# Kernel optimization log

Measured on AMD Instinct MI355X. Metric: run time of the kernel, lower is better.

The kernel has to match this reference:

```python
import jax, jax.numpy as jnp
import numpy as np

T = 8
TAU = 2.0
V_TH = 1.0
ALPHA = 2.0  # ATan surrogate alpha (spikingjelly default)

@jax.custom_vjp
def spike_fn(x):
    # Heaviside forward, ATan surrogate backward
    return (x >= 0.0).astype(x.dtype)

def _spike_fwd(x):
    return spike_fn(x), x

def _spike_bwd(x, g):
    sg = (ALPHA / 2.0) / (1.0 + (jnp.pi / 2.0 * ALPHA * x) ** 2)
    return (g * sg,)

spike_fn.defvjp(_spike_fwd, _spike_bwd)

def lif_scan(currents):
    """LIF over time. currents: (T, B, D). tau=2, v_reset=0 (hard), decay_input=True, detach_reset=True."""
    v0 = jnp.zeros(currents.shape[1:], currents.dtype)
    def step(v, x):
        v = v + (x - v) / TAU            # charge with input decay
        s = spike_fn(v - V_TH)           # fire
        sd = jax.lax.stop_gradient(s)    # detach_reset=True
        v = v * (1.0 - sd)               # hard reset to v_reset=0
        return v, s
    _, spikes = jax.lax.scan(step, v0, currents)
    return spikes  # (T, B, D)

def _linear(x, W, b):
    # x: (T,B,I), W: (O,I) torch layout
    return jnp.einsum('tbi,oi->tbo', x, W) + b

def setup_inputs() -> dict:
    key = jax.random.key(0)
    ks = jax.random.split(key, 9)
    B, D_in, D_out = 32768, 128, 64
    def lin(k, o, i):
        k1, k2 = jax.random.split(k)
        bound = 1.0 / np.sqrt(i)
        W = jax.random.uniform(k1, (o, i), jnp.float32, -bound, bound)
        b = jax.random.uniform(k2, (o,), jnp.float32, -bound, bound)
        return W, b
    W1, b1 = lin(ks[1], 256, D_in)
    W2, b2 = lin(ks[2], 128, 256)
    W3, b3 = lin(ks[3], 64, 128)
    W4, b4 = lin(ks[4], D_out, 64)
    x = jax.random.normal(ks[0], (B, D_in), jnp.float32)
    return {"x": x, "W1": W1, "b1": b1, "W2": W2, "b2": b2,
            "W3": W3, "b3": b3, "W4": W4, "b4": b4}

def reference(x, W1, b1, W2, b2, W3, b3, W4, b4):
    # Poisson rate coding: bernoulli(sigmoid(x)) per timestep (fixed key => deterministic)
    p = jax.nn.sigmoid(x)
    enc_key = jax.random.key(42)
    spikes_in = jax.random.bernoulli(enc_key, p, (T,) + x.shape).astype(x.dtype)  # (T,B,128)
    h = lif_scan(_linear(spikes_in, W1, b1))
    h = lif_scan(_linear(h, W2, b2))
    h = lif_scan(_linear(h, W3, b3))
    out = _linear(h, W4, b4)  # (T,B,64)
    return out.mean(axis=0)   # (B,64)
```

## Files before the change

kernel.cpp:

```cpp
#include <hip/hip_runtime.h>
#include <hip/hip_bf16.h>
#include <stdint.h>
#include <math.h>

#define TT 8

typedef __attribute__((ext_vector_type(8))) short short8;
typedef __attribute__((ext_vector_type(4))) float f32x4;

__device__ __forceinline__ uint16_t bf16_rne(float f) {
  uint32_t u = __float_as_uint(f);
  return (uint16_t)((u + 0x7fffu + ((u >> 16) & 1u)) >> 16);
}
__device__ __forceinline__ float bf16_f32(uint16_t b) {
  return __uint_as_float((uint32_t)b << 16);
}

__device__ __forceinline__ uint32_t rotl32(uint32_t v, int r) {
#if __has_builtin(__builtin_amdgcn_alignbit)
  return __builtin_amdgcn_alignbit(v, v, 32 - r);
#else
  return (v << r) | (v >> (32 - r));
#endif
}

__device__ __forceinline__ void tf_0_42(uint32_t x0, uint32_t x1,
                                        uint32_t& o0, uint32_t& o1) {
  const uint32_t K1 = 42u, KS2 = 0x1BD11BDAu ^ 42u;
  uint32_t v0 = x0;
  uint32_t v1 = x1 + K1;
#define R4(a,b,c,d) \
  v0 += v1; v1 = rotl32(v1, a); v1 ^= v0; \
  v0 += v1; v1 = rotl32(v1, b); v1 ^= v0; \
  v0 += v1; v1 = rotl32(v1, c); v1 ^= v0; \
  v0 += v1; v1 = rotl32(v1, d); v1 ^= v0;
  R4(13, 15, 26, 6)   v0 += K1;  v1 += KS2 + 1u;
  R4(17, 29, 16, 24)  v0 += KS2; v1 += 2u;
  R4(13, 15, 26, 6)    v1 += K1 + 3u;
  R4(17, 29, 16, 24)  v0 += K1;  v1 += KS2 + 4u;
  R4(13, 15, 26, 6)   v0 += KS2; v1 += 5u;
#undef R4
  o0 = v0; o1 = v1;
}

__device__ __forceinline__ void threefry2x32(uint32_t k0, uint32_t k1,
                                             uint32_t x0, uint32_t x1,
                                             uint32_t& o0, uint32_t& o1) {
  const uint32_t ks2 = 0x1BD11BDAu ^ k0 ^ k1;
  uint32_t v0 = x0 + k0, v1 = x1 + k1;
#define TFR(r) { v0 += v1; v1 = rotl32(v1, r); v1 ^= v0; }
  TFR(13) TFR(15) TFR(26) TFR(6)   v0 += k1;  v1 += ks2 + 1u;
  TFR(17) TFR(29) TFR(16) TFR(24)  v0 += ks2; v1 += k0 + 2u;
  TFR(13) TFR(15) TFR(26) TFR(6)   v0 += k0;  v1 += k1 + 3u;
  TFR(17) TFR(29) TFR(16) TFR(24)  v0 += k1;  v1 += ks2 + 4u;
  TFR(13) TFR(15) TFR(26) TFR(6)   v0 += ks2; v1 += k0 + 5u;
#undef TFR
  o0 = v0; o1 = v1;
}

__device__ __forceinline__ bool bern_lt(uint32_t bits, float p32, float xv) {
  const float u = __uint_as_float((bits >> 9) | 0x3f800000u) - 1.0f;
  const float d = u - p32;
  if (__builtin_expect(fabsf(d) < 8e-6f, 0)) {
    const double p = 1.0 / (1.0 + exp(-(double)xv));
    return (double)u < p;
  }
  return d < 0.0f;
}

__global__ void __launch_bounds__(256)
w1split_kernel(const float* __restrict__ W1, uint16_t* __restrict__ W1s)
{
  const int gid = blockIdx.x * 256 + threadIdx.x;
  const int j = gid & 7, nt = (gid >> 3) & 1, lane = (gid >> 4) & 63;
  const int sp = (gid >> 10) & 3, nc = gid >> 12;
  const int k = sp * 32 + (lane >> 4) * 8 + j;
  const int n = nc * 32 + nt * 16 + (lane & 15);
  W1s[gid] = bf16_rne(W1[n * 128 + k]);
}

__global__ void __launch_bounds__(256, 4)
snn_k1(const float* __restrict__ x, const uint16_t* __restrict__ W1s,
       const float* __restrict__ B1, const float* __restrict__ B4,
       uint32_t* __restrict__ s1g, uint32_t* __restrict__ flgg,
       float* __restrict__ out)
{
  __shared__ __align__(16) uint8_t sbits[128 * 16];
  __shared__ float bias_s[256];
  __shared__ uint16_t s1t[128 * 16];
  __shared__ uint32_t exc;

  const int tid = threadIdx.x;
  const int lane = tid & 63, wid = tid >> 6, g = lane >> 4;

  for (int i = tid; i < 1024; i += 256) ((uint32_t*)s1t)[i] = 0;
  if (tid == 0) exc = 0;
  bias_s[tid] = B1[tid];

  {
    const int b = tid >> 4, w8 = tid & 15;
    const int gb = blockIdx.x * 16 + b;
    float xv[8];
    *(float4*)&xv[0] = *(const float4*)&x[(size_t)gb * 128 + w8 * 8];
    *(float4*)&xv[4] = *(const float4*)&x[(size_t)gb * 128 + w8 * 8 + 4];
    const uint32_t ebase = ((uint32_t)gb << 7) | (uint32_t)(w8 * 8);
    uint32_t m[TT] = {0, 0, 0, 0, 0, 0, 0, 0};
    uint32_t ambig = 0;
    #pragma unroll
    for (int j = 0; j < 8; ++j) {
      const float p1 = 1.0f + 1.0f / (1.0f + expf(-xv[j]));
      #pragma unroll
      for (int t = 0; t < 4; ++t) {
        const uint32_t e = ebase + (uint32_t)j + ((uint32_t)t << 22);
        uint32_t o0, o1;
        tf_0_42(e, e + 0x01000000u, o0, o1);
        const float d0 = __uint_as_float((o0 >> 9) | 0x3f800000u) - p1;
        const float d1 = __uint_as_float((o1 >> 9) | 0x3f800000u) - p1;
        m[t]     |= (d0 < 0.0f ? 1u : 0u) << j;
        m[t + 4] |= (d1 < 0.0f ? 1u : 0u) << j;
        ambig |= ((fabsf(d0) < 1e-5f) || (fabsf(d1) < 1e-5f)) ? (1u << j) : 0u;
      }
    }
    if (__builtin_expect(ambig != 0u, 0)) {
      for (int j = 0; j < 8; ++j) {
        if ((ambig >> j) & 1u) {
          const double p = 1.0 / (1.0 + exp(-(double)xv[j]));
          for (int t = 0; t < 4; ++t) {
            const uint32_t e = ebase + (uint32_t)j + ((uint32_t)t << 22);
            uint32_t o0, o1;
            tf_0_42(e, e + 0x01000000u, o0, o1);
            const float u0 = __uint_as_float((o0 >> 9) | 0x3f800000u) - 1.0f;
            const float u1 = __uint_as_float((o1 >> 9) | 0x3f800000u) - 1.0f;
            m[t]     = (m[t]     & ~(1u << j)) | (((double)u0 < p ? 1u : 0u) << j);
            m[t + 4] = (m[t + 4] & ~(1u << j)) | (((double)u1 < p ? 1u : 0u) << j);
          }
        }
      }
    }
    #pragma unroll
    for (int t = 0; t < TT; ++t)
      sbits[(b * 8 + t) * 16 + w8] = (uint8_t)m[t];
  }
  __syncthreads();

  short8 a0_0, a0_1, a0_2, a0_3, a1_0, a1_1, a1_2, a1_3;
  {
    const uint8_t* rp0 = &sbits[(wid * 32 + (lane & 15)) * 16];
    const uint8_t* rp1 = rp0 + 256;
#define MKFRAG(dst, rp, s) { \
    const uint32_t byte = (rp)[(s) * 4 + g]; \
    short8 a; \
    a[0] = (short)((byte & 1u)   ? 0x3F80 : 0); \
    a[1] = (short)((byte & 2u)   ? 0x3F80 : 0); \
    a[2] = (short)((byte & 4u)   ? 0x3F80 : 0); \
    a[3] = (short)((byte & 8u)   ? 0x3F80 : 0); \
    a[4] = (short)((byte & 16u)  ? 0x3F80 : 0); \
    a[5] = (short)((byte & 32u)  ? 0x3F80 : 0); \
    a[6] = (short)((byte & 64u)  ? 0x3F80 : 0); \
    a[7] = (short)((byte & 128u) ? 0x3F80 : 0); \
    dst = a; }
    MKFRAG(a0_0, rp0, 0) MKFRAG(a0_1, rp0, 1) MKFRAG(a0_2, rp0, 2) MKFRAG(a0_3, rp0, 3)
    MKFRAG(a1_0, rp1, 0) MKFRAG(a1_1, rp1, 1) MKFRAG(a1_2, rp1, 2) MKFRAG(a1_3, rp1, 3)
#undef MKFRAG
  }

  const uint8_t* wlane = (const uint8_t*)W1s + lane * 32;

  #pragma unroll 1
  for (int nc = 0; nc < 8; ++nc) {
    const uint8_t* wnc = wlane + nc * 8192;
    f32x4 C00 = {0.f, 0.f, 0.f, 0.f};
    f32x4 C01 = C00, C10 = C00, C11 = C00;
    short8 bf0, bf1;
#define STEP(sp, A0, A1) \
    bf0 = *(const short8*)(wnc + (sp) * 2048); \
    bf1 = *(const short8*)(wnc + (sp) * 2048 + 16); \
    C00 = __builtin_amdgcn_mfma_f32_16x16x32_bf16(A0, bf0, C00, 0, 0, 0); \
    C10 = __builtin_amdgcn_mfma_f32_16x16x32_bf16(A1, bf0, C10, 0, 0, 0); \
    C01 = __builtin_amdgcn_mfma_f32_16x16x32_bf16(A0, bf1, C01, 0, 0, 0); \
    C11 = __builtin_amdgcn_mfma_f32_16x16x32_bf16(A1, bf1, C11, 0, 0, 0);
    STEP(0, a0_0, a1_0) STEP(1, a0_1, a1_1) STEP(2, a0_2, a1_2) STEP(3, a0_3, a1_3)
#undef STEP

#define EPI(Cv, mi, nt) { \
    const float bbv = bias_s[nc * 32 + (nt) * 16 + (lane & 15)]; \
    const float cr0 = Cv[0] + bbv, cr1 = Cv[1] + bbv; \
    const float cr2 = Cv[2] + bbv, cr3 = Cv[3] + bbv; \
    float u = cr0 * 0.5f; \
    float mx = u; \
    u = (u + cr1) * 0.5f; mx = fmaxf(mx, u); \
    u = (u + cr2) * 0.5f; mx = fmaxf(mx, u); \
    u = (u + cr3) * 0.5f; mx = fmaxf(mx, u); \
    const float u3o = __shfl_xor(u, 16); \
    const float ub = (g & 1) ? mx + fmaxf(u3o, 0.f) * 0.5f : mx; \
    if (__any(ub >= 1.0f)) { \
      float v = 0.f; uint32_t nib = 0; \
      { const float vn = (v + cr0) * 0.5f; const bool s = vn >= 1.0f; nib |= s ? 1u : 0u; v = s ? 0.f : vn; } \
      { const float vn = (v + cr1) * 0.5f; const bool s = vn >= 1.0f; nib |= s ? 2u : 0u; v = s ? 0.f : vn; } \
      { const float vn = (v + cr2) * 0.5f; const bool s = vn >= 1.0f; nib |= s ? 4u : 0u; v = s ? 0.f : vn; } \
      { const float vn = (v + cr3) * 0.5f; const bool s = vn >= 1.0f; nib |= s ? 8u : 0u; v = s ? 0.f : vn; } \
      const float v3 = __shfl_xor(v, 16); \
      if (g & 1) { \
        v = v3; nib = 0; \
        { const float vn = (v + cr0) * 0.5f; const bool s = vn >= 1.0f; nib |= s ? 1u : 0u; v = s ? 0.f : vn; } \
        { const float vn = (v + cr1) * 0.5f; const bool s = vn >= 1.0f; nib |= s ? 2u : 0u; v = s ? 0.f : vn; } \
        { const float vn = (v + cr2) * 0.5f; const bool s = vn >= 1.0f; nib |= s ? 4u : 0u; v = s ? 0.f : vn; } \
        { const float vn = (v + cr3) * 0.5f; const bool s = vn >= 1.0f; nib |= s ? 8u : 0u; v = s ? 0.f : vn; } \
      } \
      _Pragma("unroll") \
      for (int r = 0; r < 4; ++r) { \
        const unsigned long long bal = __ballot((nib >> r) & 1u); \
        if ((lane & 15) == 0) { \
          const uint16_t w16v = (uint16_t)((bal >> (g * 16)) & 0xffffu); \
          if (w16v) { \
            const int row = wid * 32 + (mi) * 16 + g * 4 + r; \
            s1t[row * 16 + nc * 2 + (nt)] = w16v; \
          } \
        } \
      } \
    } }
    EPI(C00, 0, 0) EPI(C01, 0, 1) EPI(C10, 1, 0) EPI(C11, 1, 1)
#undef EPI
  }

  __syncthreads();
  if (tid < 128) {
    const uint32_t* rp = (const uint32_t*)&s1t[tid * 16];
    int c = 0;
    #pragma unroll
    for (int j = 0; j < 8; ++j) c += __popc(rp[j]);
    if (c >= 15) atomicOr(&exc, 1u);
  }
  ((uint4*)s1g)[(size_t)blockIdx.x * 256 + tid] = ((const uint4*)s1t)[tid];
  __syncthreads();
  const uint32_t e = exc;
  if (tid == 0) flgg[blockIdx.x] = e;
  if (!e) {
    const float4 bv = *reinterpret_cast<const float4*>(&B4[(tid & 15) * 4]);
    float* op = &out[(size_t)(blockIdx.x * 16 + (tid >> 4)) * 64 + (tid & 15) * 4];
    *reinterpret_cast<float4*>(op) = bv;
  }
}

template<int I, int O, bool LAST>
__device__ __forceinline__ void layer_valu(
    const float* __restrict__ Wg, const float* __restrict__ Bg,
    const uint32_t* __restrict__ s_in, uint8_t* __restrict__ s_out,
    uint32_t* __restrict__ flg_next,
    float* __restrict__ wbuf, float* __restrict__ bias_s,
    float* __restrict__ outp, int bglob0, uint32_t msk)
{
  constexpr int WST = 66;
  const int tid = threadIdx.x;
  const int b  = tid >> 3;
  const int oc = tid & 7;
  __syncthreads();
  if (tid < O) bias_s[tid] = Bg[tid];

  for (int q = 0; q < O / 64; ++q) {
    const int obase = q * 64;
    float acc[TT][8];
    #pragma unroll
    for (int t = 0; t < TT; ++t)
      #pragma unroll
      for (int j = 0; j < 8; ++j) acc[t][j] = 0.f;

    for (int ic = 0; ic < I / 64; ++ic) {
      if (!((msk >> ic) & 1u)) continue;
      __syncthreads();
      #pragma unroll
      for (int k = 0; k < 4; ++k) {
        int fi = tid + k * 256;
        int o  = fi >> 4;
        int i4 = fi & 15;
        const float4 w4 = *reinterpret_cast<const float4*>(
            &Wg[(size_t)(obase + o) * I + ic * 64 + i4 * 4]);
        float* wp = &wbuf[(i4 * 4) * WST + o];
        wp[0 * WST] = w4.x; wp[1 * WST] = w4.y;
        wp[2 * WST] = w4.z; wp[3 * WST] = w4.w;
      }
      __syncthreads();
      uint32_t r[TT][2];
      uint32_t any = 0;
      #pragma unroll
      for (int t = 0; t < TT; ++t) {
        const uint32_t* sp = &s_in[(size_t)(b * 8 + t) * (I / 32) + ic * 2];
        r[t][0] = sp[0]; r[t][1] = sp[1];
        any |= r[t][0] | r[t][1];
      }
      if (any) {
        #pragma unroll
        for (int w = 0; w < 2; ++w) {
          for (int i2 = 0; i2 < 32; ++i2) {
            const float* wrow = &wbuf[(w * 32 + i2) * WST + oc * 8];
            const float2 wa = *reinterpret_cast<const float2*>(wrow);
            const float2 wb = *reinterpret_cast<const float2*>(wrow + 2);
            const float2 wc = *reinterpret_cast<const float2*>(wrow + 4);
            const float2 wd = *reinterpret_cast<const float2*>(wrow + 6);
            #pragma unroll
            for (int t = 0; t < TT; ++t) {
              const float sf = (float)((r[t][w] >> i2) & 1u);
              acc[t][0] += wa.x * sf; acc[t][1] += wa.y * sf;
              acc[t][2] += wb.x * sf; acc[t][3] += wb.y * sf;
              acc[t][4] += wc.x * sf; acc[t][5] += wc.y * sf;
              acc[t][6] += wd.x * sf; acc[t][7] += wd.y * sf;
            }
          }
        }
      }
    }
    if constexpr (!LAST) {
      float v[8];
      #pragma unroll
      for (int j = 0; j < 8; ++j) v[j] = 0.f;
      #pragma unroll
      for (int t = 0; t < TT; ++t) {
        uint32_t m = 0;
        #pragma unroll
        for (int j = 0; j < 8; ++j) {
          const float cur = acc[t][j] + bias_s[obase + oc * 8 + j];
          const float vn = (v[j] + cur) * 0.5f;
          const bool s = vn >= 1.0f;
          m |= (uint32_t)s << j;
          v[j] = s ? 0.0f : vn;
        }
        if (m) {
          const int byi = (obase >> 3) + oc;
          s_out[(size_t)(b * 8 + t) * (O / 8) + byi] = (uint8_t)m;
          atomicOr(flg_next, 1u << (byi >> 3));
        }
      }
    } else {
      float oacc[8];
      #pragma unroll
      for (int j = 0; j < 8; ++j) oacc[j] = 0.f;
      #pragma unroll
      for (int t = 0; t < TT; ++t)
        #pragma unroll
        for (int j = 0; j < 8; ++j) oacc[j] += acc[t][j];
      float4 o0, o1;
      o0.x = oacc[0] * 0.125f + bias_s[oc * 8 + 0];
      o0.y = oacc[1] * 0.125f + bias_s[oc * 8 + 1];
      o0.z = oacc[2] * 0.125f + bias_s[oc * 8 + 2];
      o0.w = oacc[3] * 0.125f + bias_s[oc * 8 + 3];
      o1.x = oacc[4] * 0.125f + bias_s[oc * 8 + 4];
      o1.y = oacc[5] * 0.125f + bias_s[oc * 8 + 5];
      o1.z = oacc[6] * 0.125f + bias_s[oc * 8 + 6];
      o1.w = oacc[7] * 0.125f + bias_s[oc * 8 + 7];
      float* op = &outp[(size_t)(bglob0 + b) * 64 + oc * 8];
      *reinterpret_cast<float4*>(op)     = o0;
      *reinterpret_cast<float4*>(op + 4) = o1;
    }
  }
}

__global__ void __launch_bounds__(256, 4)
snn_k2(const uint32_t* __restrict__ s1g, const uint32_t* __restrict__ flgg,
       const float* __restrict__ W2, const float* __restrict__ B2,
       const float* __restrict__ W3, const float* __restrict__ B3,
       const float* __restrict__ W4, const float* __restrict__ B4,
       float* __restrict__ out)
{
  const uint32_t m1 = flgg[2 * blockIdx.x] | flgg[2 * blockIdx.x + 1];
  if (!m1) return;

  __shared__ __align__(16) uint8_t smem[32272];
  float*    wbuf   = (float*)smem;
  float*    bias_s = (float*)(smem + 16896);
  uint8_t*  s2     = smem + 17920;
  uint32_t* s1     = (uint32_t*)(smem + 22016);
  uint8_t*  s3     = smem + 30208;
  uint32_t* flg    = (uint32_t*)(smem + 32256);

  const int tid = threadIdx.x;
  const int bglob0 = blockIdx.x * 32;

  ((uint4*)s1)[tid]       = ((const uint4*)s1g)[(size_t)blockIdx.x * 512 + tid];
  ((uint4*)s1)[tid + 256] = ((const uint4*)s1g)[(size_t)blockIdx.x * 512 + tid + 256];
  for (int i = tid; i < 1024; i += 256) ((uint32_t*)s2)[i] = 0;
  for (int i = tid; i < 516;  i += 256) ((uint32_t*)s3)[i] = 0;

  layer_valu<256, 128, false>(W2, B2, s1, s2, &flg[1],
                              wbuf, bias_s, nullptr, bglob0, 0xFu);
  __syncthreads();
  const uint32_t m2 = flg[1];
  if (m2)
    layer_valu<128, 64, false>(W3, B3, (const uint32_t*)s2, s3, &flg[2],
                               wbuf, bias_s, nullptr, bglob0, m2);
  __syncthreads();
  const uint32_t m3 = flg[2];
  if (m3) {
    layer_valu<64, 64, true>(W4, B4, (const uint32_t*)s3, nullptr, nullptr,
                             wbuf, bias_s, out, bglob0, m3);
  } else {
    const int b = tid >> 3, oc = tid & 7;
    const float4 b0 = *reinterpret_cast<const float4*>(&B4[oc * 8]);
    const float4 b1 = *reinterpret_cast<const float4*>(&B4[oc * 8 + 4]);
    float* op = &out[(size_t)(bglob0 + b) * 64 + oc * 8];
    *reinterpret_cast<float4*>(op)     = b0;
    *reinterpret_cast<float4*>(op + 4) = b1;
  }
}

__global__ void __launch_bounds__(256, 4)
snn_fb(const float* __restrict__ x,
       const float* __restrict__ W1, const float* __restrict__ B1,
       const float* __restrict__ W2, const float* __restrict__ B2,
       const float* __restrict__ W3, const float* __restrict__ B3,
       const float* __restrict__ W4, const float* __restrict__ B4,
       float* __restrict__ out)
{
  __shared__ __align__(16) uint8_t smem[32272];
  uint16_t* B_lds  = (uint16_t*)smem;
  float*    wbuf   = (float*)smem;
  float*    bias_s = (float*)(smem + 16896);
  uint32_t* s0     = (uint32_t*)(smem + 17920);
  uint8_t*  s2     = smem + 17920;
  uint16_t* s1     = (uint16_t*)(smem + 22016);
  uint8_t*  s3     = smem + 30208;
  uint32_t* flg    = (uint32_t*)(smem + 32256);

  const int tid = threadIdx.x;
  const int lane = tid & 63, wid = tid >> 6;
  const int bglob0 = blockIdx.x * 32;

  for (int i = tid; i < 2564; i += 256)
    ((uint32_t*)(smem + 22016))[i] = 0;

  {
    const int b = tid >> 3, w16 = tid & 7;
    const int gb = bglob0 + b;
    float xv[16];
    #pragma unroll
    for (int k = 0; k < 4; ++k)
      *(float4*)&xv[k * 4] =
          *(const float4*)&x[(size_t)gb * 128 + w16 * 16 + k * 4];
    uint32_t m[TT] = {0, 0, 0, 0, 0, 0, 0, 0};
    for (int j = 0; j < 16; ++j) {
      const int d = w16 * 16 + j;
      const float p32 = 1.0f / (1.0f + expf(-xv[j]));
      #pragma unroll
      for (int t = 0; t < 4; ++t) {
        const uint32_t e = ((uint32_t)t << 22) | ((uint32_t)gb << 7) | (uint32_t)d;
        uint32_t o0, o1;
        threefry2x32(0u, 42u, e, e + 0x01000000u, o0, o1);
        m[t]     |= (uint32_t)bern_lt(o0, p32, xv[j]) << j;
        m[t + 4] |= (uint32_t)bern_lt(o1, p32, xv[j]) << j;
      }
    }
    #pragma unroll
    for (int t = 0; t < TT; ++t)
      ((uint16_t*)s0)[(b * 8 + t) * 8 + w16] = (uint16_t)m[t];
  }
  bias_s[tid] = B1[tid];
  __syncthreads();

  short8 afrag[4][4];
  #pragma unroll
  for (int m = 0; m < 4; ++m) {
    const int row = wid * 64 + m * 16 + (lane & 15);
    #pragma unroll
    for (int s = 0; s < 4; ++s) {
      const uint32_t wrd = s0[row * 4 + s];
      const uint32_t byte = (wrd >> ((lane >> 4) * 8)) & 0xffu;
      short8 a;
      #pragma unroll
      for (int j = 0; j < 8; ++j)
        a[j] = (short)(((byte >> j) & 1u) ? 0x3F80 : 0);
      afrag[m][s] = a;
    }
  }
  __syncthreads();
  for (int i = tid; i < 1024; i += 256)
    ((uint32_t*)s2)[i] = 0;

  for (int nc = 0; nc < 8; ++nc) {
    __syncthreads();
    {
      const int col = tid >> 3, kq = tid & 7;
      const float* wsrc = &W1[(size_t)(nc * 32 + col) * 128 + kq * 16];
      float4 f[4];
      #pragma unroll
      for (int k = 0; k < 4; ++k)
        f[k] = *reinterpret_cast<const float4*>(wsrc + k * 4);
      #pragma unroll
      for (int h = 0; h < 2; ++h) {
        const int k0 = kq * 16 + h * 8;
        const int sp = k0 >> 5, gg = (k0 >> 3) & 3;
        short8 hv, lv;
        #pragma unroll
        for (int e = 0; e < 8; ++e) {
          const float w = ((const float*)&f[2 * h])[e];
          const uint16_t hb = bf16_rne(w);
          const uint16_t lb = bf16_rne(w - bf16_f32(hb));
          hv[e] = (short)hb; lv[e] = (short)lb;
        }
        *(short8*)(B_lds + ((sp * 4 + gg) * 33 + col) * 8)       = hv;
        *(short8*)(B_lds + (((sp + 4) * 4 + gg) * 33 + col) * 8) = lv;
      }
    }
    __syncthreads();
    f32x4 C[4][2];
    #pragma unroll
    for (int m = 0; m < 4; ++m)
      #pragma unroll
      for (int nt = 0; nt < 2; ++nt)
        C[m][nt] = (f32x4){0.f, 0.f, 0.f, 0.f};
    #pragma unroll
    for (int nt = 0; nt < 2; ++nt)
      #pragma unroll
      for (int sp = 0; sp < 8; ++sp) {
        const short8 bf = *(const short8*)(
            B_lds + ((sp * 4 + (lane >> 4)) * 33 + nt * 16 + (lane & 15)) * 8);
        #pragma unroll
        for (int m = 0; m < 4; ++m)
          C[m][nt] = __builtin_amdgcn_mfma_f32_16x16x32_bf16(
              afrag[m][sp & 3], bf, C[m][nt], 0, 0, 0);
      }
    const int g = lane >> 4;
    #pragma unroll
    for (int m = 0; m < 4; ++m)
      #pragma unroll
      for (int nt = 0; nt < 2; ++nt) {
        const float bb = bias_s[nc * 32 + nt * 16 + (lane & 15)];
        const float c0 = C[m][nt][0] + bb, c1 = C[m][nt][1] + bb;
        const float c2 = C[m][nt][2] + bb, c3 = C[m][nt][3] + bb;
        const float mxc = fmaxf(fmaxf(c0, c1), fmaxf(c2, c3));
        if (__any(mxc >= 1.0f)) {
          float cr[4] = {c0, c1, c2, c3};
          float v = 0.f; uint32_t nib = 0;
          #pragma unroll
          for (int r = 0; r < 4; ++r) {
            const float vn = (v + cr[r]) * 0.5f;
            const bool s = vn >= 1.0f;
            nib |= (uint32_t)s << r;
            v = s ? 0.f : vn;
          }
          const float v3 = __shfl_xor(v, 16);
          if (g & 1) {
            v = v3; nib = 0;
            #pragma unroll
            for (int r = 0; r < 4; ++r) {
              const float vn = (v + cr[r]) * 0.5f;
              const bool s = vn >= 1.0f;
              nib |= (uint32_t)s << r;
              v = s ? 0.f : vn;
            }
          }
          #pragma unroll
          for (int r = 0; r < 4; ++r) {
            const unsigned long long bal = __ballot((nib >> r) & 1u);
            if ((lane & 15) == 0) {
              const uint16_t w16v = (uint16_t)((bal >> (g * 16)) & 0xffffu);
              if (w16v) {
                const int row = wid * 64 + m * 16 + g * 4 + r;
                const int wds = nc * 2 + nt;
                s1[row * 16 + wds] = w16v;
                atomicOr(&flg[0], 1u << (wds >> 2));
              }
            }
          }
        }
      }
  }

  __syncthreads();
  const uint32_t m1 = flg[0];
  if (m1)
    layer_valu<256, 128, false>(W2, B2, (const uint32_t*)s1, s2, &flg[1],
                                wbuf, bias_s, nullptr, bglob0, m1);
  __syncthreads();
  const uint32_t m2 = flg[1];
  if (m2)
    layer_valu<128, 64, false>(W3, B3, (const uint32_t*)s2, s3, &flg[2],
                               wbuf, bias_s, nullptr, bglob0, m2);
  __syncthreads();
  const uint32_t m3 = flg[2];
  if (m3) {
    layer_valu<64, 64, true>(W4, B4, (const uint32_t*)s3, nullptr, nullptr,
                             wbuf, bias_s, out, bglob0, m3);
  } else {
    const int b = tid >> 3, oc = tid & 7;
    const float4 b0 = *reinterpret_cast<const float4*>(&B4[oc * 8]);
    const float4 b1 = *reinterpret_cast<const float4*>(&B4[oc * 8 + 4]);
    float* op = &out[(size_t)(bglob0 + b) * 64 + oc * 8];
    *reinterpret_cast<float4*>(op)     = b0;
    *reinterpret_cast<float4*>(op + 4) = b1;
  }
}

extern "C" void kernel_launch(void* const* d_in, const int* in_sizes, int n_in,
                              void* d_out, int out_size, void* d_ws, size_t ws_size,
                              hipStream_t stream) {
  const float* x  = (const float*)d_in[0];
  const float* W1 = (const float*)d_in[1];
  const float* B1 = (const float*)d_in[2];
  const float* W2 = (const float*)d_in[3];
  const float* B2 = (const float*)d_in[4];
  const float* W3 = (const float*)d_in[5];
  const float* B3 = (const float*)d_in[6];
  const float* W4 = (const float*)d_in[7];
  const float* B4 = (const float*)d_in[8];
  float* out = (float*)d_out;
  const size_t s1_bytes  = (size_t)262144 * 32;
  const size_t flg_bytes = 2048 * 4;
  const size_t w1s_bytes = 32768 * 2;
  if (ws_size >= s1_bytes + flg_bytes + w1s_bytes) {
    uint32_t* s1g  = (uint32_t*)d_ws;
    uint32_t* flgg = (uint32_t*)((uint8_t*)d_ws + s1_bytes);
    uint16_t* W1s  = (uint16_t*)((uint8_t*)d_ws + s1_bytes + flg_bytes);
    hipLaunchKernelGGL(w1split_kernel, dim3(128), dim3(256), 0, stream, W1, W1s);
    hipLaunchKernelGGL(snn_k1, dim3(2048), dim3(256), 0, stream,
                       x, W1s, B1, B4, s1g, flgg, out);
    hipLaunchKernelGGL(snn_k2, dim3(1024), dim3(256), 0, stream,
                       s1g, flgg, W2, B2, W3, B3, W4, B4, out);
  } else {
    hipLaunchKernelGGL(snn_fb, dim3(1024), dim3(256), 0, stream,
                       x, W1, B1, W2, B2, W3, B3, W4, B4, out);
  }
}
```

Baseline: 77.59 us.

## Split Poisson encoding into a separate kernel writing packed spike bits

Moves the Threefry-based Bernoulli encoding out of snn_k1 into a new enc2_kernel that uses twice as many threads (4 elements per thread instead of 8) and writes packed spike bytes to a workspace buffer. snn_k1b then just loads those bits into shared memory before its MFMA layer-1 work. This aims to relieve register pressure and raise parallelism for the RNG-heavy phase, and to let the GEMM kernel run leaner. The cost is an extra kernel launch, a larger workspace requirement, and a global round-trip of 4 MB of spike bits.

```diff
diff --git a/kernel.cpp b/kernel.cpp
--- a/kernel.cpp
+++ b/kernel.cpp
@@ -36,7 +36,7 @@
   v0 += v1; v1 = rotl32(v1, d); v1 ^= v0;
   R4(13, 15, 26, 6)   v0 += K1;  v1 += KS2 + 1u;
   R4(17, 29, 16, 24)  v0 += KS2; v1 += 2u;
-  R4(13, 15, 26, 6)    v1 += K1 + 3u;
+  R4(13, 15, 26, 6)   v1 += K1 + 3u;
   R4(17, 29, 16, 24)  v0 += K1;  v1 += KS2 + 4u;
   R4(13, 15, 26, 6)   v0 += KS2; v1 += 5u;
 #undef R4
@@ -79,11 +79,65 @@
   W1s[gid] = bf16_rne(W1[n * 128 + k]);
 }
 
+__global__ void __launch_bounds__(256)
+enc2_kernel(const float* __restrict__ x, uint32_t* __restrict__ s0g)
+{
+  __shared__ uint8_t sb[64 * 16];
+  const int tid = threadIdx.x;
+  const int b = tid >> 5, q = tid & 31;
+  const int gb = blockIdx.x * 8 + b;
+  const float4 xv4 = *(const float4*)&x[(size_t)gb * 128 + q * 4];
+  const float xv[4] = {xv4.x, xv4.y, xv4.z, xv4.w};
+  const uint32_t ebase = ((uint32_t)gb << 7) | (uint32_t)(q * 4);
+  uint32_t m[TT] = {0, 0, 0, 0, 0, 0, 0, 0};
+  uint32_t ambig = 0;
+  #pragma unroll
+  for (int j = 0; j < 4; ++j) {
+    const float p1 = 1.0f + 1.0f / (1.0f + expf(-xv[j]));
+    #pragma unroll
+    for (int t = 0; t < 4; ++t) {
+      const uint32_t e = ebase + (uint32_t)j + ((uint32_t)t << 22);
+      uint32_t o0, o1;
+      tf_0_42(e, e + 0x01000000u, o0, o1);
+      const float d0 = __uint_as_float((o0 >> 9) | 0x3f800000u) - p1;
+      const float d1 = __uint_as_float((o1 >> 9) | 0x3f800000u) - p1;
+      m[t]     |= (d0 < 0.0f ? 1u : 0u) << j;
+      m[t + 4] |= (d1 < 0.0f ? 1u : 0u) << j;
+      ambig |= ((fabsf(d0) < 1e-5f) || (fabsf(d1) < 1e-5f)) ? (1u << j) : 0u;
+    }
+  }
+  if (__builtin_expect(ambig != 0u, 0)) {
+    for (int j = 0; j < 4; ++j) {
+      if ((ambig >> j) & 1u) {
+        const double p = 1.0 / (1.0 + exp(-(double)xv[j]));
+        for (int t = 0; t < 4; ++t) {
+          const uint32_t e = ebase + (uint32_t)j + ((uint32_t)t << 22);
+          uint32_t o0, o1;
+          tf_0_42(e, e + 0x01000000u, o0, o1);
+          const float u0 = __uint_as_float((o0 >> 9) | 0x3f800000u) - 1.0f;
+          const float u1 = __uint_as_float((o1 >> 9) | 0x3f800000u) - 1.0f;
+          m[t]     = (m[t]     & ~(1u << j)) | (((double)u0 < p ? 1u : 0u) << j);
+          m[t + 4] = (m[t + 4] & ~(1u << j)) | (((double)u1 < p ? 1u : 0u) << j);
+        }
+      }
+    }
+  }
+  #pragma unroll
+  for (int t = 0; t < TT; ++t) {
+    const uint32_t other = (uint32_t)__shfl_xor((int)m[t], 1);
+    if (!(q & 1))
+      sb[(b * 8 + t) * 16 + (q >> 1)] = (uint8_t)(m[t] | (other << 4));
+  }
+  __syncthreads();
+  if (tid < 64)
+    ((uint4*)s0g)[(size_t)blockIdx.x * 64 + tid] = ((const uint4*)sb)[tid];
+}
+
 __global__ void __launch_bounds__(256, 4)
-snn_k1(const float* __restrict__ x, const uint16_t* __restrict__ W1s,
-       const float* __restrict__ B1, const float* __restrict__ B4,
-       uint32_t* __restrict__ s1g, uint32_t* __restrict__ flgg,
-       float* __restrict__ out)
+snn_k1b(const uint32_t* __restrict__ s0g, const uint16_t* __restrict__ W1s,
+        const float* __restrict__ B1, const float* __restrict__ B4,
+        uint32_t* __restrict__ s1g, uint32_t* __restrict__ flgg,
+        float* __restrict__ out)
 {
   __shared__ __align__(16) uint8_t sbits[128 * 16];
   __shared__ float bias_s[256];
@@ -96,51 +150,8 @@
   for (int i = tid; i < 1024; i += 256) ((uint32_t*)s1t)[i] = 0;
   if (tid == 0) exc = 0;
   bias_s[tid] = B1[tid];
-
-  {
-    const int b = tid >> 4, w8 = tid & 15;
-    const int gb = blockIdx.x * 16 + b;
-    float xv[8];
-    *(float4*)&xv[0] = *(const float4*)&x[(size_t)gb * 128 + w8 * 8];
-    *(float4*)&xv[4] = *(const float4*)&x[(size_t)gb * 128 + w8 * 8 + 4];
-    const uint32_t ebase = ((uint32_t)gb << 7) | (uint32_t)(w8 * 8);
-    uint32_t m[TT] = {0, 0, 0, 0, 0, 0, 0, 0};
-    uint32_t ambig = 0;
-    #pragma unroll
-    for (int j = 0; j < 8; ++j) {
-      const float p1 = 1.0f + 1.0f / (1.0f + expf(-xv[j]));
-      #pragma unroll
-      for (int t = 0; t < 4; ++t) {
-        const uint32_t e = ebase + (uint32_t)j + ((uint32_t)t << 22);
-        uint32_t o0, o1;
-        tf_0_42(e, e + 0x01000000u, o0, o1);
-        const float d0 = __uint_as_float((o0 >> 9) | 0x3f800000u) - p1;
-        const float d1 = __uint_as_float((o1 >> 9) | 0x3f800000u) - p1;
-        m[t]     |= (d0 < 0.0f ? 1u : 0u) << j;
-        m[t + 4] |= (d1 < 0.0f ? 1u : 0u) << j;
-        ambig |= ((fabsf(d0) < 1e-5f) || (fabsf(d1) < 1e-5f)) ? (1u << j) : 0u;
-      }
-    }
-    if (__builtin_expect(ambig != 0u, 0)) {
-      for (int j = 0; j < 8; ++j) {
-        if ((ambig >> j) & 1u) {
-          const double p = 1.0 / (1.0 + exp(-(double)xv[j]));
-          for (int t = 0; t < 4; ++t) {
-            const uint32_t e = ebase + (uint32_t)j + ((uint32_t)t << 22);
-            uint32_t o0, o1;
-            tf_0_42(e, e + 0x01000000u, o0, o1);
-            const float u0 = __uint_as_float((o0 >> 9) | 0x3f800000u) - 1.0f;
-            const float u1 = __uint_as_float((o1 >> 9) | 0x3f800000u) - 1.0f;
-            m[t]     = (m[t]     & ~(1u << j)) | (((double)u0 < p ? 1u : 0u) << j);
-            m[t + 4] = (m[t + 4] & ~(1u << j)) | (((double)u1 < p ? 1u : 0u) << j);
-          }
-        }
-      }
-    }
-    #pragma unroll
-    for (int t = 0; t < TT; ++t)
-      sbits[(b * 8 + t) * 16 + w8] = (uint8_t)m[t];
-  }
+  if (tid < 128)
+    ((uint4*)sbits)[tid] = ((const uint4*)s0g)[(size_t)blockIdx.x * 128 + tid];
   __syncthreads();
 
   short8 a0_0, a0_1, a0_2, a0_3, a1_0, a1_1, a1_2, a1_3;
@@ -605,13 +616,17 @@
   const size_t s1_bytes  = (size_t)262144 * 32;
   const size_t flg_bytes = 2048 * 4;
   const size_t w1s_bytes = 32768 * 2;
-  if (ws_size >= s1_bytes + flg_bytes + w1s_bytes) {
-    uint32_t* s1g  = (uint32_t*)d_ws;
-    uint32_t* flgg = (uint32_t*)((uint8_t*)d_ws + s1_bytes);
-    uint16_t* W1s  = (uint16_t*)((uint8_t*)d_ws + s1_bytes + flg_bytes);
+  const size_t s0_bytes  = (size_t)32768 * 8 * 16;
+  if (ws_size >= s1_bytes + flg_bytes + w1s_bytes + s0_bytes) {
+    uint8_t* wsb = (uint8_t*)d_ws;
+    uint32_t* s1g  = (uint32_t*)wsb;
+    uint32_t* flgg = (uint32_t*)(wsb + s1_bytes);
+    uint16_t* W1s  = (uint16_t*)(wsb + s1_bytes + flg_bytes);
+    uint32_t* s0g  = (uint32_t*)(wsb + s1_bytes + flg_bytes + w1s_bytes);
     hipLaunchKernelGGL(w1split_kernel, dim3(128), dim3(256), 0, stream, W1, W1s);
-    hipLaunchKernelGGL(snn_k1, dim3(2048), dim3(256), 0, stream,
-                       x, W1s, B1, B4, s1g, flgg, out);
+    hipLaunchKernelGGL(enc2_kernel, dim3(4096), dim3(256), 0, stream, x, s0g);
+    hipLaunchKernelGGL(snn_k1b, dim3(2048), dim3(256), 0, stream,
+                       s0g, W1s, B1, B4, s1g, flgg, out);
     hipLaunchKernelGGL(snn_k2, dim3(1024), dim3(256), 0, stream,
                        s1g, flgg, W2, B2, W3, B3, W4, B4, out);
   } else {
```

Result: slower. 86.43 us (+11.4%).
